# Optimization experiments

Hardware: AMD Instinct MI355X
Metric: run time of the kernel (lower is better)

Reference implementation:

```python
import jax, jax.numpy as jnp
import numpy as np

D_MODEL = 1024


def setup_inputs() -> dict:
    key = jax.random.key(0)
    k1, k2, k3, k4, k5, k6 = jax.random.split(key, 6)
    B, S, D = 4, 4096, D_MODEL
    scale = 1.0 / np.sqrt(D)
    return {
        "hidden": jax.random.normal(k1, (B, S, D), dtype=jnp.float32),
        "pre_emb": jax.random.normal(k2, (B, S, D), dtype=jnp.float32),
        "w1": jax.random.normal(k3, (D, D), dtype=jnp.float32) * scale,  # [in, out]
        "b1": jax.random.normal(k4, (D,), dtype=jnp.float32) * 0.01,
        "w2": jax.random.normal(k5, (D, D), dtype=jnp.float32) * scale,
        "b2": jax.random.normal(k6, (D,), dtype=jnp.float32) * 0.01,
    }


def reference(hidden, pre_emb, w1, b1, w2, b2):
    # h = Linear1(hidden); i = Linear2(hidden + pre_emb)
    h = jnp.einsum("bsd,de->bse", hidden, w1) + b1            # [B,S,D]
    i = jnp.einsum("bsd,de->bse", hidden + pre_emb, w2) + b2  # [B,S,D]
    attn = jnp.einsum("bqd,bkd->bqk", h, i)                   # [B,S,S]
    return jax.nn.softmax(attn, axis=-1)
```

## Files before the change

### kernel.cpp

```cpp
#include <hip/hip_runtime.h>
#include <hip/hip_bf16.h>
#include <stdint.h>

#define DM   1024
#define BATCH 4
#define SEQ  4096
#define MTOT (BATCH*SEQ)

typedef __attribute__((ext_vector_type(8))) short bf16x8;
typedef __attribute__((ext_vector_type(4))) float f32x4;
typedef __attribute__((ext_vector_type(16))) float f32x16;

#define GLOAD_LDS16(gp, lp) __builtin_amdgcn_global_load_lds( \
    (const __attribute__((address_space(1))) unsigned int*)(gp), \
    (__attribute__((address_space(3))) unsigned int*)(lp), 16, 0, 0)

#define VMCNT(n) asm volatile("s_waitcnt vmcnt(" #n ")" ::: "memory")
#define BAR()    __builtin_amdgcn_s_barrier()
#define FENCE()  asm volatile("" ::: "memory")

__device__ __forceinline__ ushort f2bf(float f){
  uint u = __float_as_uint(f);
  u += 0x7FFFu + ((u >> 16) & 1u);
  return (ushort)(u >> 16);
}
__device__ __forceinline__ float bf2f(ushort b){ return __uint_as_float(((uint)b) << 16); }

__device__ __forceinline__ void split4(const float4 v, ushort4& h4, ushort4& l4){
  h4.x = f2bf(v.x); l4.x = f2bf(v.x - bf2f(h4.x));
  h4.y = f2bf(v.y); l4.y = f2bf(v.y - bf2f(h4.y));
  h4.z = f2bf(v.z); l4.z = f2bf(v.z - bf2f(h4.z));
  h4.w = f2bf(v.w); l4.w = f2bf(v.w - bf2f(h4.w));
}

__global__ __launch_bounds__(256)
void prep_w_split(const float* __restrict__ w1, const float* __restrict__ w2,
                  ushort* __restrict__ w1h, ushort* __restrict__ w1l,
                  ushort* __restrict__ w2h, ushort* __restrict__ w2l){
  const float* w = blockIdx.y ? w2 : w1;
  ushort* oh = blockIdx.y ? w2h : w1h;
  ushort* ol = blockIdx.y ? w2l : w1l;
  size_t off = ((size_t)blockIdx.x * 256 + threadIdx.x) * 4;
  float4 v = *(const float4*)&w[off];
  ushort4 h4, l4; split4(v, h4, l4);
  *(ushort4*)&oh[off] = h4;
  *(ushort4*)&ol[off] = l4;
}

__global__ __launch_bounds__(256)
void prep_xy(const float* __restrict__ hidden, const float* __restrict__ pre,
             ushort* __restrict__ xh, ushort* __restrict__ xl,
             ushort* __restrict__ yh, ushort* __restrict__ yl,
             const float* __restrict__ c2, float* __restrict__ beta, int writeX){
  __shared__ float red[4];
  const int tid = threadIdx.x, lane = tid & 63, wid = tid >> 6;
  size_t off = ((size_t)blockIdx.x * 256 + tid) * 4;
  float4 h = *(const float4*)&hidden[off];
  float4 p = *(const float4*)&pre[off];
  float4 y = {h.x + p.x, h.y + p.y, h.z + p.z, h.w + p.w};
  ushort4 a, b;
  if (writeX){
    split4(h, a, b);
    *(ushort4*)&xh[off] = a;
    *(ushort4*)&xl[off] = b;
  }
  split4(y, a, b);
  *(ushort4*)&yh[off] = a;
  *(ushort4*)&yl[off] = b;

  float4 c = *(const float4*)&c2[tid * 4];
  float s = y.x * c.x + y.y * c.y + y.z * c.z + y.w * c.w;
  #pragma unroll
  for (int o = 32; o > 0; o >>= 1) s += __shfl_xor(s, o, 64);
  if (lane == 0) red[wid] = s;
  __syncthreads();
  if (tid == 0) beta[blockIdx.x] = red[0] + red[1] + red[2] + red[3];
}

__global__ __launch_bounds__(256)
void c2k(const float* __restrict__ w2, const float* __restrict__ b1,
         float* __restrict__ c2){
  const int wid = threadIdx.x >> 6, lane = threadIdx.x & 63;
  const int row = blockIdx.x * 4 + wid;
  float s = 0.f;
  #pragma unroll
  for (int t = 0; t < 16; t++){
    int e = lane + 64 * t;
    s += w2[(size_t)row * DM + e] * b1[e];
  }
  #pragma unroll
  for (int o = 32; o > 0; o >>= 1) s += __shfl_xor(s, o, 64);
  if (lane == 0) c2[row] = s;
}

__device__ __forceinline__ void mainloop256(
    const ushort* __restrict__ Aph, const ushort* __restrict__ Apl,
    const ushort* __restrict__ Bph, const ushort* __restrict__ Bpl,
    int m0, int n0, f32x16 (&acc)[4][2]){
  __shared__ alignas(16) ushort lds[2][4][256*32];

  const int tid = threadIdx.x;
  const int lane = tid & 63, wv = tid >> 6;
  const int wm = (wv & 1) * 128, wn = (wv >> 1) * 64;
  const int l31 = lane & 31;
  const int skey2 = ((lane >> 1) & 3) ^ (((lane >> 4) & 1) << 1);
  const int offk0 = ((((lane >> 5) + 0) ^ skey2) << 3);
  const int offk1 = ((((lane >> 5) + 2) ^ skey2) << 3);

  const int rowidx = tid >> 2;
  const int srcc = ((((tid & 3) ^ ((tid >> 3) & 3)) ^ (((tid >> 6) & 1) << 1)) << 3);
  const int arow = rowidx + (rowidx & 64);
  const int brow = ((rowidx >> 5) << 6) + (rowidx & 31);
  const int awrow = wv * 16 + ((wv & 4) << 4);
  const int bwrow = ((wv >> 1) << 6) + ((wv & 1) << 4);

  auto stageA = [&](int bf, int qa, int kt){
    const size_t g = (size_t)(m0 + qa * 64 + arow) * DM + kt * 32 + srcc;
    GLOAD_LDS16(Aph + g, &lds[bf][0][(qa * 64 + awrow) * 32]);
    GLOAD_LDS16(Apl + g, &lds[bf][1][(qa * 64 + awrow) * 32]);
  };
  auto stageB = [&](int bf, int qb, int kt){
    const size_t g = (size_t)(n0 + qb * 32 + brow) * DM + kt * 32 + srcc;
    GLOAD_LDS16(Bph + g, &lds[bf][2][(qb * 32 + bwrow) * 32]);
    GLOAD_LDS16(Bpl + g, &lds[bf][3][(qb * 32 + bwrow) * 32]);
  };

  bf16x8 ah[2][2], al[2][2];
  bf16x8 bh0[2], bl0[2], bh1[2], bl1[2];

#define DS_A32(CUR, QA) do { _Pragma("unroll") for (int blk = 0; blk < 2; blk++){ \
    ah[blk][0] = *(const bf16x8*)&lds[CUR][0][(wm + (QA)*64 + blk*32 + l31)*32 + offk0]; \
    ah[blk][1] = *(const bf16x8*)&lds[CUR][0][(wm + (QA)*64 + blk*32 + l31)*32 + offk1]; \
    al[blk][0] = *(const bf16x8*)&lds[CUR][1][(wm + (QA)*64 + blk*32 + l31)*32 + offk0]; \
    al[blk][1] = *(const bf16x8*)&lds[CUR][1][(wm + (QA)*64 + blk*32 + l31)*32 + offk1]; } } while(0)
#define DS_B32(CUR, QB, BH, BL) do { \
    BH[0] = *(const bf16x8*)&lds[CUR][2][(wn + (QB)*32 + l31)*32 + offk0]; \
    BH[1] = *(const bf16x8*)&lds[CUR][2][(wn + (QB)*32 + l31)*32 + offk1]; \
    BL[0] = *(const bf16x8*)&lds[CUR][3][(wn + (QB)*32 + l31)*32 + offk0]; \
    BL[1] = *(const bf16x8*)&lds[CUR][3][(wn + (QB)*32 + l31)*32 + offk1]; } while(0)
#define MFMA32(QA, QB, BH, BL) do { \
  __builtin_amdgcn_s_setprio(1); \
  _Pragma("unroll") for (int ks = 0; ks < 2; ks++) _Pragma("unroll") for (int blk = 0; blk < 2; blk++) \
    acc[(QA)*2+blk][QB] = __builtin_amdgcn_mfma_f32_32x32x16_bf16(ah[blk][ks], BH[ks], acc[(QA)*2+blk][QB], 0, 0, 0); \
  _Pragma("unroll") for (int ks = 0; ks < 2; ks++) _Pragma("unroll") for (int blk = 0; blk < 2; blk++) \
    acc[(QA)*2+blk][QB] = __builtin_amdgcn_mfma_f32_32x32x16_bf16(ah[blk][ks], BL[ks], acc[(QA)*2+blk][QB], 0, 0, 0); \
  _Pragma("unroll") for (int ks = 0; ks < 2; ks++) _Pragma("unroll") for (int blk = 0; blk < 2; blk++) \
    acc[(QA)*2+blk][QB] = __builtin_amdgcn_mfma_f32_32x32x16_bf16(al[blk][ks], BH[ks], acc[(QA)*2+blk][QB], 0, 0, 0); \
  __builtin_amdgcn_s_setprio(0); } while(0)

  stageA(0, 0, 0); stageB(0, 0, 0); stageB(0, 1, 0); stageA(0, 1, 0);

  for (int t = 0; t < 31; ++t){
    const int cur = t & 1, nxt = cur ^ 1;
    VMCNT(4); BAR(); FENCE();
    DS_A32(cur, 0); DS_B32(cur, 0, bh0, bl0);
    stageA(nxt, 0, t + 1);
    MFMA32(0, 0, bh0, bl0);
    BAR();
    VMCNT(4); BAR(); FENCE();
    DS_B32(cur, 1, bh1, bl1);
    stageB(nxt, 0, t + 1);
    MFMA32(0, 1, bh1, bl1);
    BAR();
    VMCNT(4); BAR(); FENCE();
    DS_A32(cur, 1);
    stageB(nxt, 1, t + 1);
    MFMA32(1, 1, bh1, bl1);
    BAR();
    stageA(nxt, 1, t + 1);
    MFMA32(1, 0, bh0, bl0);
    BAR();
  }
  {
    VMCNT(4); BAR(); FENCE();
    DS_A32(1, 0); DS_B32(1, 0, bh0, bl0);
    MFMA32(0, 0, bh0, bl0);
    BAR();
    VMCNT(2); BAR(); FENCE();
    DS_B32(1, 1, bh1, bl1);
    MFMA32(0, 1, bh1, bl1);
    BAR();
    VMCNT(0); BAR(); FENCE();
    DS_A32(1, 1);
    MFMA32(1, 1, bh1, bl1);
    BAR();
    MFMA32(1, 0, bh0, bl0);
  }
#undef DS_A32
#undef DS_B32
#undef MFMA32
}

__global__ __launch_bounds__(512, 2)
void gemm_bt_split256(const ushort* __restrict__ Aph, const ushort* __restrict__ Apl,
                      const ushort* __restrict__ Bph, const ushort* __restrict__ Bpl,
                      ushort* __restrict__ oh, ushort* __restrict__ ol){
  const int m0 = blockIdx.y * 256, n0 = blockIdx.x * 256;
  f32x16 acc[4][2] = {};
  mainloop256(Aph, Apl, Bph, Bpl, m0, n0, acc);

  const int tid = threadIdx.x, lane = tid & 63, wv = tid >> 6;
  const int wm = (wv & 1) * 128, wn = (wv >> 1) * 64;
  const int l31 = lane & 31, rup = (lane >> 5) * 4;
  #pragma unroll
  for (int I = 0; I < 4; I++)
    #pragma unroll
    for (int J = 0; J < 2; J++){
      int gc = n0 + wn + J*32 + l31;
      #pragma unroll
      for (int r = 0; r < 16; r++){
        int gr = m0 + wm + I*32 + (r & 3) + 8*(r >> 2) + rup;
        float v = acc[I][J][r];
        ushort hb = f2bf(v);
        size_t o = (size_t)gr * DM + gc;
        oh[o] = hb;
        ol[o] = f2bf(v - bf2f(hb));
      }
    }
}

__global__ __launch_bounds__(512, 2)
void gemm_bt_f32_256(const ushort* __restrict__ Aph, const ushort* __restrict__ Apl,
                     const ushort* __restrict__ Bph, const ushort* __restrict__ Bpl,
                     float* __restrict__ out){
  const int b = blockIdx.y;
  const int id = blockIdx.x;
  const int c = id & 7;
  const int m = id >> 3;
  const int qt = (c >> 1) * 4 + (m >> 3);
  const int kt = (c & 1) * 8 + (m & 7);
  const int m0 = qt * 256, n0 = kt * 256;
  const size_t abase = (size_t)b * SEQ * DM;

  f32x16 acc[4][2] = {};
  mainloop256(Aph + abase, Apl + abase, Bph + abase, Bpl + abase, m0, n0, acc);

  const int tid = threadIdx.x, lane = tid & 63, wv = tid >> 6;
  const int wm = (wv & 1) * 128, wn = (wv >> 1) * 64;
  const int l31 = lane & 31, rup = (lane >> 5) * 4;
  #pragma unroll
  for (int I = 0; I < 4; I++)
    #pragma unroll
    for (int J = 0; J < 2; J++){
      int gc = n0 + wn + J*32 + l31;
      #pragma unroll
      for (int r = 0; r < 16; r++){
        int gr = m0 + wm + I*32 + (r & 3) + 8*(r >> 2) + rup;
        __builtin_nontemporal_store(acc[I][J][r],
            &out[((size_t)b * SEQ + gr) * SEQ + gc]);
      }
    }
}

__device__ __forceinline__ void bt_mainloop(
    const ushort* __restrict__ Aph, const ushort* __restrict__ Apl,
    const ushort* __restrict__ Bph, const ushort* __restrict__ Bpl,
    int m0, int n0, f32x4 (&acc)[4][4]){
  __shared__ alignas(16) ushort Ah[128*32];
  __shared__ alignas(16) ushort Al[128*32];
  __shared__ alignas(16) ushort Bh[128*32];
  __shared__ alignas(16) ushort Bl[128*32];

  const int tid = threadIdx.x;
  const int lane = tid & 63, wid = tid >> 6;
  const int wm = (wid & 1) * 64, wn = (wid >> 1) * 64;
  const int lr = lane & 15;
  const int lks = (((lane >> 4) ^ ((lane >> 1) & 3)) << 3);

  const ushort* plane = (wid == 0) ? Aph : (wid == 1) ? Apl : (wid == 2) ? Bph : Bpl;
  ushort* lds = (wid == 0) ? Ah : (wid == 1) ? Al : (wid == 2) ? Bh : Bl;
  const int r0 = (wid < 2) ? m0 : n0;
  const size_t goff = (size_t)(r0 + (lane >> 2)) * DM
                    + (size_t)(((lane & 3) ^ ((lane >> 3) & 3)) * 8);

  for (int k0 = 0; k0 < DM; k0 += 32){
    __syncthreads();
    const ushort* gp = plane + goff + k0;
    #pragma unroll
    for (int t = 0; t < 8; t++){
      GLOAD_LDS16(gp + (size_t)t * 16 * DM, lds + t * 512);
    }
    __syncthreads();

    bf16x8 fah[4], fal[4], fbh[4], fbl[4];
    #pragma unroll
    for (int i = 0; i < 4; i++){
      fah[i] = *(const bf16x8*)&Ah[(wm + i*16 + lr)*32 + lks];
      fal[i] = *(const bf16x8*)&Al[(wm + i*16 + lr)*32 + lks];
      fbh[i] = *(const bf16x8*)&Bh[(wn + i*16 + lr)*32 + lks];
      fbl[i] = *(const bf16x8*)&Bl[(wn + i*16 + lr)*32 + lks];
    }
    #pragma unroll
    for (int i = 0; i < 4; i++)
      #pragma unroll
      for (int j = 0; j < 4; j++){
        acc[i][j] = __builtin_amdgcn_mfma_f32_16x16x32_bf16(fah[i], fbh[j], acc[i][j], 0, 0, 0);
        acc[i][j] = __builtin_amdgcn_mfma_f32_16x16x32_bf16(fah[i], fbl[j], acc[i][j], 0, 0, 0);
        acc[i][j] = __builtin_amdgcn_mfma_f32_16x16x32_bf16(fal[i], fbh[j], acc[i][j], 0, 0, 0);
      }
  }
}

__global__ __launch_bounds__(256, 2)
void gemm_bt_split(const ushort* __restrict__ Aph, const ushort* __restrict__ Apl,
                   const ushort* __restrict__ Bph, const ushort* __restrict__ Bpl,
                   ushort* __restrict__ oh, ushort* __restrict__ ol){
  const int m0 = blockIdx.y * 128, n0 = blockIdx.x * 128;
  f32x4 acc[4][4];
  for (int i = 0; i < 4; i++) for (int j = 0; j < 4; j++) acc[i][j] = (f32x4){0.f,0.f,0.f,0.f};
  bt_mainloop(Aph, Apl, Bph, Bpl, m0, n0, acc);

  const int lane = threadIdx.x & 63, wid = threadIdx.x >> 6;
  const int wm = (wid & 1) * 64, wn = (wid >> 1) * 64;
  const int lr = lane & 15;
  const int rbase = (lane >> 4) * 4;
  #pragma unroll
  for (int i = 0; i < 4; i++)
    #pragma unroll
    for (int j = 0; j < 4; j++){
      int gc = n0 + wn + j*16 + lr;
      #pragma unroll
      for (int r = 0; r < 4; r++){
        int gr = m0 + wm + i*16 + rbase + r;
        float v = acc[i][j][r];
        ushort hb = f2bf(v);
        size_t o = (size_t)gr * DM + gc;
        oh[o] = hb;
        ol[o] = f2bf(v - bf2f(hb));
      }
    }
}

#define ASTR 40
__global__ __launch_bounds__(256, 2)
void gemm_z_manual(const float* __restrict__ hidden,
                   const ushort* __restrict__ gth, const ushort* __restrict__ gtl,
                   ushort* __restrict__ zh, ushort* __restrict__ zl){
  const int m0 = blockIdx.y * 128, n0 = blockIdx.x * 128;
  __shared__ alignas(16) ushort Ah[128*ASTR];
  __shared__ alignas(16) ushort Al[128*ASTR];
  __shared__ alignas(16) ushort Bh[128*32];
  __shared__ alignas(16) ushort Bl[128*32];

  const int tid = threadIdx.x;
  const int lane = tid & 63, wid = tid >> 6;
  const int wm = (wid & 1) * 64, wn = (wid >> 1) * 64;
  const int lr = lane & 15, lk = (lane >> 4) * 8;
  const int lks = (((lane >> 4) ^ ((lane >> 1) & 3)) << 3);

  const ushort* bp = (wid < 2) ? gth : gtl;
  ushort* blds = (wid < 2) ? Bh : Bl;
  const int tb = (wid & 1) * 4;
  const size_t bgoff = (size_t)(n0 + (lane >> 2)) * DM
                     + (size_t)(((lane & 3) ^ ((lane >> 3) & 3)) * 8);

  f32x4 acc[4][4];
  for (int i = 0; i < 4; i++) for (int j = 0; j < 4; j++) acc[i][j] = (f32x4){0.f,0.f,0.f,0.f};

  for (int k0 = 0; k0 < DM; k0 += 32){
    __syncthreads();
    const ushort* gb = bp + bgoff + k0;
    #pragma unroll
    for (int t = 0; t < 4; t++){
      GLOAD_LDS16(gb + (size_t)(tb + t) * 16 * DM, blds + (tb + t) * 512);
    }
    #pragma unroll
    for (int c = 0; c < 4; c++){
      int idx = c * 256 + tid;
      int row = idx >> 3, kq = (idx & 7) * 4;
      size_t ga = (size_t)(m0 + row) * DM + k0 + kq;
      float4 v = *(const float4*)&hidden[ga];
      ushort4 h4, l4;
      split4(v, h4, l4);
      *(ushort4*)&Ah[row*ASTR + kq] = h4;
      *(ushort4*)&Al[row*ASTR + kq] = l4;
    }
    __syncthreads();

    bf16x8 fah[4], fal[4], fbh[4], fbl[4];
    #pragma unroll
    for (int i = 0; i < 4; i++){
      fah[i] = *(const bf16x8*)&Ah[(wm + i*16 + lr)*ASTR + lk];
      fal[i] = *(const bf16x8*)&Al[(wm + i*16 + lr)*ASTR + lk];
      fbh[i] = *(const bf16x8*)&Bh[(wn + i*16 + lr)*32 + lks];
      fbl[i] = *(const bf16x8*)&Bl[(wn + i*16 + lr)*32 + lks];
    }
    #pragma unroll
    for (int i = 0; i < 4; i++)
      #pragma unroll
      for (int j = 0; j < 4; j++){
        acc[i][j] = __builtin_amdgcn_mfma_f32_16x16x32_bf16(fah[i], fbh[j], acc[i][j], 0, 0, 0);
        acc[i][j] = __builtin_amdgcn_mfma_f32_16x16x32_bf16(fah[i], fbl[j], acc[i][j], 0, 0, 0);
        acc[i][j] = __builtin_amdgcn_mfma_f32_16x16x32_bf16(fal[i], fbh[j], acc[i][j], 0, 0, 0);
      }
  }

  const int rbase = (lane >> 4) * 4;
  #pragma unroll
  for (int i = 0; i < 4; i++)
    #pragma unroll
    for (int j = 0; j < 4; j++){
      int gc = n0 + wn + j*16 + lr;
      #pragma unroll
      for (int r = 0; r < 4; r++){
        int gr = m0 + wm + i*16 + rbase + r;
        float v = acc[i][j][r];
        ushort hb = f2bf(v);
        size_t o = (size_t)gr * DM + gc;
        zh[o] = hb;
        zl[o] = f2bf(v - bf2f(hb));
      }
    }
}

__global__ __launch_bounds__(256)
void softmax_rows(float* __restrict__ out, const float* __restrict__ beta){
  __shared__ float red[8];
  const size_t row = blockIdx.x;
  float* p = out + row * (size_t)SEQ;
  const float* bp = beta + ((row >> 12) << 12);
  const int tid = threadIdx.x, lane = tid & 63, wid = tid >> 6;

  f32x4 v[4];
  float m = -3.0e38f;
  #pragma unroll
  for (int c = 0; c < 4; c++){
    v[c] = __builtin_nontemporal_load(((const f32x4*)p) + c*256 + tid);
    f32x4 bb = *(((const f32x4*)bp) + c*256 + tid);
    v[c] += bb;
    m = fmaxf(m, fmaxf(fmaxf(v[c].x, v[c].y), fmaxf(v[c].z, v[c].w)));
  }
  #pragma unroll
  for (int o = 32; o > 0; o >>= 1) m = fmaxf(m, __shfl_xor(m, o, 64));
  if (lane == 0) red[wid] = m;
  __syncthreads();
  const float M = fmaxf(fmaxf(red[0], red[1]), fmaxf(red[2], red[3]));

  float s = 0.f;
  #pragma unroll
  for (int c = 0; c < 4; c++){
    v[c].x = __expf(v[c].x - M); s += v[c].x;
    v[c].y = __expf(v[c].y - M); s += v[c].y;
    v[c].z = __expf(v[c].z - M); s += v[c].z;
    v[c].w = __expf(v[c].w - M); s += v[c].w;
  }
  #pragma unroll
  for (int o = 32; o > 0; o >>= 1) s += __shfl_xor(s, o, 64);
  if (lane == 0) red[4 + wid] = s;
  __syncthreads();
  const float inv = 1.0f / (red[4] + red[5] + red[6] + red[7]);
  #pragma unroll
  for (int c = 0; c < 4; c++){
    v[c] *= inv;
    __builtin_nontemporal_store(v[c], ((f32x4*)p) + c*256 + tid);
  }
}

extern "C" void kernel_launch(void* const* d_in, const int* in_sizes, int n_in,
                              void* d_out, int out_size, void* d_ws, size_t ws_size,
                              hipStream_t stream){
  const float* hidden = (const float*)d_in[0];
  const float* pre    = (const float*)d_in[1];
  const float* w1     = (const float*)d_in[2];
  const float* b1     = (const float*)d_in[3];
  const float* w2     = (const float*)d_in[4];
  float* out = (float*)d_out;

  char* ws = (char*)d_ws;
  const size_t WP = (size_t)DM * DM * sizeof(ushort);
  const size_t AP = (size_t)MTOT * DM * sizeof(ushort);
  const bool big = ws_size >= 6*AP + 6*WP + (1u << 20);

  ushort *w1h, *w1l, *w2h, *w2l, *Gth, *Gtl, *Xh, *Xl, *Yh, *Yl, *Zh, *Zl;
  float *c2, *beta;
  if (big){
    Xh  = (ushort*)(ws + 0*AP);  Xl  = (ushort*)(ws + 1*AP);
    Yh  = (ushort*)(ws + 2*AP);  Yl  = (ushort*)(ws + 3*AP);
    Zh  = (ushort*)(ws + 4*AP);  Zl  = (ushort*)(ws + 5*AP);
    w1h = (ushort*)(ws + 6*AP);          w1l = (ushort*)(ws + 6*AP + WP);
    w2h = (ushort*)(ws + 6*AP + 2*WP);   w2l = (ushort*)(ws + 6*AP + 3*WP);
    Gth = (ushort*)(ws + 6*AP + 4*WP);   Gtl = (ushort*)(ws + 6*AP + 5*WP);
    c2   = (float*)(ws + 6*AP + 6*WP);
    beta = c2 + DM;
  } else {
    Zh  = (ushort*)(ws + 0*AP);  Zl  = (ushort*)(ws + 1*AP);
    Yh  = (ushort*)(ws + 2*AP);  Yl  = (ushort*)(ws + 3*AP);
    Gth = (ushort*)(ws + 4*AP);  Gtl = (ushort*)(ws + 4*AP + WP);
    w1h = (ushort*)(ws + 0);       w1l = (ushort*)(ws + WP);
    w2h = (ushort*)(ws + 2*WP);    w2l = (ushort*)(ws + 3*WP);
    c2   = (float*)(ws + 4*AP + 2*WP);
    beta = c2 + DM;
    Xh = Xl = nullptr;
  }

  prep_w_split<<<dim3(1024, 2), 256, 0, stream>>>(w1, w2, w1h, w1l, w2h, w2l);
  c2k<<<dim3(256), 256, 0, stream>>>(w2, b1, c2);
  prep_xy<<<dim3(16384), 256, 0, stream>>>(hidden, pre, Xh, Xl, Yh, Yl, c2, beta, big ? 1 : 0);
  gemm_bt_split<<<dim3(8, 8), 256, 0, stream>>>(w2h, w2l, w1h, w1l, Gth, Gtl);
  if (big){
    gemm_bt_split256<<<dim3(4, 64), 512, 0, stream>>>(Xh, Xl, Gth, Gtl, Zh, Zl);
  } else {
    gemm_z_manual<<<dim3(8, 128), 256, 0, stream>>>(hidden, Gth, Gtl, Zh, Zl);
  }
  gemm_bt_f32_256<<<dim3(256, BATCH), 512, 0, stream>>>(Zh, Zl, Yh, Yl, out);
  softmax_rows<<<dim3(MTOT), 256, 0, stream>>>(out, beta);
}
```

Before: 918.5 us.

## Store LDS tiles in MFMA-fragment order instead of swizzled row-major

Changes the shared-memory layout of the A/B tiles so each global_load_lds writes data directly in the order each lane reads for MFMA operands, replacing the XOR-swizzled row-major layout. LDS reads become contiguous per lane group (lane-linear 16-byte chunks), which aims to remove bank conflicts and address arithmetic. Global loads now fetch 16-byte chunks from 32 distinct rows per wave, which may reduce global coalescing.

```diff
diff --git a/kernel.cpp b/kernel.cpp
--- a/kernel.cpp
+++ b/kernel.cpp
@@ -101,43 +101,44 @@
 
   const int tid = threadIdx.x;
   const int lane = tid & 63, wv = tid >> 6;
-  const int wm = (wv & 1) * 128, wn = (wv >> 1) * 64;
   const int l31 = lane & 31;
-  const int skey2 = ((lane >> 1) & 3) ^ (((lane >> 4) & 1) << 1);
-  const int offk0 = ((((lane >> 5) + 0) ^ skey2) << 3);
-  const int offk1 = ((((lane >> 5) + 2) ^ skey2) << 3);
-
-  const int rowidx = tid >> 2;
-  const int srcc = ((((tid & 3) ^ ((tid >> 3) & 3)) ^ (((tid >> 6) & 1) << 1)) << 3);
-  const int arow = rowidx + (rowidx & 64);
-  const int brow = ((rowidx >> 5) << 6) + (rowidx & 31);
-  const int awrow = wv * 16 + ((wv & 4) << 4);
-  const int bwrow = ((wv >> 1) << 6) + ((wv & 1) << 4);
+
+  const int rdoff  = (lane >> 5) * 256 + l31 * 8;
+  const int agbase = (wv & 1) * 4;
+  const int bgbase = (wv >> 1) * 2;
+
+  const int kcOff    = ((wv & 1) * 2 + (lane >> 5)) * 8;
+  const int aRowBase = (wv >> 2) * 128 + ((wv >> 1) & 1) * 32 + l31;
+  const int bRowBase = (wv >> 1) * 64 + l31;
+  const int aDst     = (wv >> 2) * 4096 + (wv & 3) * 512;
+  const int bDst     = (wv >> 1) * 2048 + (wv & 1) * 512;
 
   auto stageA = [&](int bf, int qa, int kt){
-    const size_t g = (size_t)(m0 + qa * 64 + arow) * DM + kt * 32 + srcc;
-    GLOAD_LDS16(Aph + g, &lds[bf][0][(qa * 64 + awrow) * 32]);
-    GLOAD_LDS16(Apl + g, &lds[bf][1][(qa * 64 + awrow) * 32]);
+    const size_t g = (size_t)(m0 + qa * 64 + aRowBase) * DM + kt * 32 + kcOff;
+    GLOAD_LDS16(Aph + g, &lds[bf][0][qa * 2048 + aDst]);
+    GLOAD_LDS16(Apl + g, &lds[bf][1][qa * 2048 + aDst]);
   };
   auto stageB = [&](int bf, int qb, int kt){
-    const size_t g = (size_t)(n0 + qb * 32 + brow) * DM + kt * 32 + srcc;
-    GLOAD_LDS16(Bph + g, &lds[bf][2][(qb * 32 + bwrow) * 32]);
-    GLOAD_LDS16(Bpl + g, &lds[bf][3][(qb * 32 + bwrow) * 32]);
+    const size_t g = (size_t)(n0 + qb * 32 + bRowBase) * DM + kt * 32 + kcOff;
+    GLOAD_LDS16(Bph + g, &lds[bf][2][qb * 1024 + bDst]);
+    GLOAD_LDS16(Bpl + g, &lds[bf][3][qb * 1024 + bDst]);
   };
 
   bf16x8 ah[2][2], al[2][2];
   bf16x8 bh0[2], bl0[2], bh1[2], bl1[2];
 
 #define DS_A32(CUR, QA) do { _Pragma("unroll") for (int blk = 0; blk < 2; blk++){ \
-    ah[blk][0] = *(const bf16x8*)&lds[CUR][0][(wm + (QA)*64 + blk*32 + l31)*32 + offk0]; \
-    ah[blk][1] = *(const bf16x8*)&lds[CUR][0][(wm + (QA)*64 + blk*32 + l31)*32 + offk1]; \
-    al[blk][0] = *(const bf16x8*)&lds[CUR][1][(wm + (QA)*64 + blk*32 + l31)*32 + offk0]; \
-    al[blk][1] = *(const bf16x8*)&lds[CUR][1][(wm + (QA)*64 + blk*32 + l31)*32 + offk1]; } } while(0)
+    const int gA = (agbase + (QA)*2 + blk) * 1024; \
+    ah[blk][0] = *(const bf16x8*)&lds[CUR][0][gA + rdoff]; \
+    ah[blk][1] = *(const bf16x8*)&lds[CUR][0][gA + 512 + rdoff]; \
+    al[blk][0] = *(const bf16x8*)&lds[CUR][1][gA + rdoff]; \
+    al[blk][1] = *(const bf16x8*)&lds[CUR][1][gA + 512 + rdoff]; } } while(0)
 #define DS_B32(CUR, QB, BH, BL) do { \
-    BH[0] = *(const bf16x8*)&lds[CUR][2][(wn + (QB)*32 + l31)*32 + offk0]; \
-    BH[1] = *(const bf16x8*)&lds[CUR][2][(wn + (QB)*32 + l31)*32 + offk1]; \
-    BL[0] = *(const bf16x8*)&lds[CUR][3][(wn + (QB)*32 + l31)*32 + offk0]; \
-    BL[1] = *(const bf16x8*)&lds[CUR][3][(wn + (QB)*32 + l31)*32 + offk1]; } while(0)
+    const int gB = (bgbase + (QB)) * 1024; \
+    BH[0] = *(const bf16x8*)&lds[CUR][2][gB + rdoff]; \
+    BH[1] = *(const bf16x8*)&lds[CUR][2][gB + 512 + rdoff]; \
+    BL[0] = *(const bf16x8*)&lds[CUR][3][gB + rdoff]; \
+    BL[1] = *(const bf16x8*)&lds[CUR][3][gB + 512 + rdoff]; } while(0)
 #define MFMA32(QA, QB, BH, BL) do { \
   __builtin_amdgcn_s_setprio(1); \
   _Pragma("unroll") for (int ks = 0; ks < 2; ks++) _Pragma("unroll") for (int blk = 0; blk < 2; blk++) \
```

Result: no change. 913.8 us (-0.5%).
